# Optimization experiments

Hardware: AMD Instinct MI355X
Metric: run time of the kernel (lower is better)

The kernel has to match this reference:

```python
import jax, jax.numpy as jnp
import numpy as np

N_NODES = 100000
N_EDGES = 1250000
NUM_SKILLS = 100000
HID = 64


def _sage(h, src, dst, Wl, bl, Wr, n):
    # SAGEConv (PyG defaults): out = lin_l(mean_{j in N(i)} h_j) + lin_r(h_i)
    msgs = h[src]                                        # [E, d] gather
    agg = jax.ops.segment_sum(msgs, dst, num_segments=n)  # [N, d]
    cnt = jax.ops.segment_sum(jnp.ones((src.shape[0],), h.dtype), dst, num_segments=n)
    mean = agg / jnp.maximum(cnt, 1.0)[:, None]
    return mean @ Wl + bl + h @ Wr


def _prelu(v, a):
    return jnp.where(v >= 0, v, a * v)


def setup_inputs() -> dict:
    key = jax.random.key(0)
    ks = jax.random.split(key, 12)
    s = 1.0 / np.sqrt(HID)
    inp = {
        "x": jax.random.randint(ks[0], (N_NODES,), 0, NUM_SKILLS),
        "edge_index": jax.random.randint(ks[1], (2, N_EDGES), 0, N_NODES),
        "edge_weight": jax.random.uniform(ks[2], (N_EDGES,), jnp.float32),
        "emb": jax.random.normal(ks[3], (NUM_SKILLS, HID), jnp.float32),
        "Wl1": jax.random.uniform(ks[4], (HID, HID), jnp.float32, -s, s),
        "bl1": jnp.zeros((HID,), jnp.float32),
        "Wr1": jax.random.uniform(ks[5], (HID, HID), jnp.float32, -s, s),
        "a1": jnp.float32(0.25),
        "Wl2": jax.random.uniform(ks[6], (HID, HID), jnp.float32, -s, s),
        "bl2": jnp.zeros((HID,), jnp.float32),
        "Wr2": jax.random.uniform(ks[7], (HID, HID), jnp.float32, -s, s),
        "a2": jnp.float32(0.25),
        "Wout": jax.random.uniform(ks[8], (HID, HID), jnp.float32, -s, s),
        "bout": jnp.zeros((HID,), jnp.float32),
    }
    return inp


def reference(x, edge_index, edge_weight, emb, Wl1, bl1, Wr1, a1,
              Wl2, bl2, Wr2, a2, Wout, bout):
    src, dst = edge_index[0], edge_index[1]
    n = x.shape[0]
    h0 = emb[x]                                           # [N, d] embedding lookup
    h1 = _prelu(_sage(h0, src, dst, Wl1, bl1, Wr1, n), a1)  # dropout = identity (eval)
    h2 = _prelu(_sage(h1, src, dst, Wl2, bl2, Wr2, n), a2)
    return h2 @ Wout + bout
```

## Files before the change

### kernel.cpp

```cpp
#include <hip/hip_runtime.h>
#include <hip/hip_bf16.h>

#define N_NODES 100000
#define N_EDGES 1250000
#define HID 64
#define LDSS 72
#define NB 196
#define NBLOCK 128
#define EMB_BLOCKS 6250

typedef __bf16 bf16x8 __attribute__((ext_vector_type(8)));
typedef float  f32x4  __attribute__((ext_vector_type(4)));

__device__ __forceinline__ float bflo(uint u) {
    union { unsigned int i; float f; } v; v.i = u << 16; return v.f;
}
__device__ __forceinline__ float bfhi(uint u) {
    union { unsigned int i; float f; } v; v.i = u & 0xFFFF0000u; return v.f;
}
__device__ __forceinline__ ushort f2bf(float f) {
    union { float f; unsigned int i; } v; v.f = f;
    unsigned int x = v.i;
    return (ushort)((x + 0x7fffu + ((x >> 16) & 1u)) >> 16);
}

__global__ __launch_bounds__(256) void prep(const int* __restrict__ x,
                                            const float* __restrict__ emb,
                                            ushort* __restrict__ h0,
                                            const int* __restrict__ dst,
                                            int* __restrict__ gh,
                                            const float* __restrict__ Wl1,
                                            const float* __restrict__ Wr1,
                                            const float* __restrict__ Wl2,
                                            const float* __restrict__ Wr2,
                                            const float* __restrict__ Wout,
                                            ushort* __restrict__ wbf) {
    const int b = blockIdx.x;
    const int tid = threadIdx.x;
    if (b < EMB_BLOCKS) {
        int t = b * 256 + tid;
        int row = t >> 4, c = t & 15;
        int idx = x[row];
        float4 v = ((const float4*)(emb + (size_t)idx * HID))[c];
        ushort4 w;
        w.x = f2bf(v.x); w.y = f2bf(v.y); w.z = f2bf(v.z); w.w = f2bf(v.w);
        ((ushort4*)(h0 + (size_t)row * HID))[c] = w;
    } else if (b < EMB_BLOCKS + NBLOCK) {
        __shared__ int hist[NB];
        const int bb = b - EMB_BLOCKS;
        for (int i = tid; i < NB; i += 256) hist[i] = 0;
        __syncthreads();
        const int4* d4 = (const int4*)dst;
        for (int e = bb * 256 + tid; e < N_EDGES / 4; e += NBLOCK * 256) {
            int4 v = d4[e];
            atomicAdd(&hist[v.x >> 9], 1);
            atomicAdd(&hist[v.y >> 9], 1);
            atomicAdd(&hist[v.z >> 9], 1);
            atomicAdd(&hist[v.w >> 9], 1);
        }
        __syncthreads();
        for (int i = tid; i < NB; i += 256) gh[bb * NB + i] = hist[i];
    } else {
        const int wb = b - EMB_BLOCKS - NBLOCK;
        const float* W = (wb == 0) ? Wl1 : (wb == 1) ? Wr1 :
                         (wb == 2) ? Wl2 : (wb == 3) ? Wr2 : Wout;
        ushort* o = wbf + wb * 4096;
        for (int idx = tid; idx < 4096; idx += 256) {
            int k = idx >> 6, n = idx & 63;
            o[n * 64 + k] = f2bf(W[idx]);
        }
    }
}

__global__ __launch_bounds__(256) void p3_scatter(const int* __restrict__ src,
                                                  const int* __restrict__ dst,
                                                  const int* __restrict__ gh,
                                                  int* __restrict__ bstart,
                                                  uint* __restrict__ ebuf) {
    __shared__ int base[NB];
    __shared__ int run[NB];
    __shared__ int wsum[4];
    const int tid = threadIdx.x, lane = tid & 63, wave = tid >> 6;
    int myTot = 0, myPre = 0;
    if (tid < NB) {
        for (int b = 0; b < NBLOCK; ++b) {
            int c = gh[b * NB + tid];
            if (b == (int)blockIdx.x) myPre = myTot;
            myTot += c;
        }
    }
    int x = myTot;
#pragma unroll
    for (int d = 1; d < 64; d <<= 1) {
        int y = __shfl_up(x, d, 64);
        if (lane >= d) x += y;
    }
    if (lane == 63) wsum[wave] = x;
    __syncthreads();
    if (wave == 0) {
        int s = (lane < 4) ? wsum[lane] : 0;
#pragma unroll
        for (int d = 1; d < 4; d <<= 1) {
            int y = __shfl_up(s, d, 64);
            if (lane >= d) s += y;
        }
        if (lane < 4) wsum[lane] = s;
    }
    __syncthreads();
    int waveoff = (wave == 0) ? 0 : wsum[wave - 1];
    int excl = waveoff + (x - myTot);
    if (tid < NB) {
        base[tid] = excl + myPre;
        run[tid] = 0;
        if (blockIdx.x == 0) bstart[tid] = excl;
    }
    if (blockIdx.x == 0 && tid == 0) bstart[NB] = N_EDGES;
    __syncthreads();
    const int4* s4 = (const int4*)src;
    const int4* d4 = (const int4*)dst;
    for (int e = blockIdx.x * 256 + tid; e < N_EDGES / 4; e += NBLOCK * 256) {
        int4 dv = d4[e];
        int4 sv = s4[e];
        int b0 = dv.x >> 9;
        int r0 = atomicAdd(&run[b0], 1);
        ebuf[base[b0] + r0] = ((uint)(dv.x & 511) << 17) | (uint)sv.x;
        int b1 = dv.y >> 9;
        int r1 = atomicAdd(&run[b1], 1);
        ebuf[base[b1] + r1] = ((uint)(dv.y & 511) << 17) | (uint)sv.y;
        int b2 = dv.z >> 9;
        int r2 = atomicAdd(&run[b2], 1);
        ebuf[base[b2] + r2] = ((uint)(dv.z & 511) << 17) | (uint)sv.z;
        int b3 = dv.w >> 9;
        int r3 = atomicAdd(&run[b3], 1);
        ebuf[base[b3] + r3] = ((uint)(dv.w & 511) << 17) | (uint)sv.w;
    }
}

__global__ __launch_bounds__(256) void p4_csr(const uint* __restrict__ ebuf,
                                              const int* __restrict__ bstart,
                                              int* __restrict__ rowptr,
                                              int* __restrict__ csr_src) {
    __shared__ int hist[512], hoff[512], run[512];
    __shared__ int wsum[4];
    const int v = blockIdx.x;
    const int tid = threadIdx.x, lane = tid & 63, wave = tid >> 6;
    const int node0 = v << 9;
    const int nn = min(512, N_NODES - node0);
    const int beg = bstart[v], end = bstart[v + 1];

    for (int i = tid; i < 512; i += 256) { hist[i] = 0; run[i] = 0; }
    __syncthreads();
    for (int e = beg + tid; e < end; e += 256)
        atomicAdd(&hist[ebuf[e] >> 17], 1);
    __syncthreads();
    int h0 = hist[2 * tid], h1 = hist[2 * tid + 1];
    int s = h0 + h1;
    int x = s;
#pragma unroll
    for (int d = 1; d < 64; d <<= 1) {
        int y = __shfl_up(x, d, 64);
        if (lane >= d) x += y;
    }
    if (lane == 63) wsum[wave] = x;
    __syncthreads();
    if (wave == 0) {
        int s2 = (lane < 4) ? wsum[lane] : 0;
#pragma unroll
        for (int d = 1; d < 4; d <<= 1) {
            int y = __shfl_up(s2, d, 64);
            if (lane >= d) s2 += y;
        }
        if (lane < 4) wsum[lane] = s2;
    }
    __syncthreads();
    int waveoff = (wave == 0) ? 0 : wsum[wave - 1];
    int excl = waveoff + (x - s);
    hoff[2 * tid] = excl;
    hoff[2 * tid + 1] = excl + h0;
    __syncthreads();
    for (int j = tid; j < nn; j += 256) rowptr[node0 + j] = beg + hoff[j];
    if (v == NB - 1 && tid == 0) rowptr[N_NODES] = N_EDGES;
    for (int e = beg + tid; e < end; e += 256) {
        uint p = ebuf[e];
        int dl = p >> 17;
        int r = atomicAdd(&run[dl], 1);
        csr_src[beg + hoff[dl] + r] = (int)(p & 0x1FFFFu);
    }
}

#define ACCUM(wa, wb)                                                      \
    a0 += bflo(wa.x); a1 += bfhi(wa.x); a2 += bflo(wa.y); a3 += bfhi(wa.y); \
    a4 += bflo(wa.z); a5 += bfhi(wa.z); a6 += bflo(wa.w); a7 += bfhi(wa.w); \
    a8 += bflo(wb.x); a9 += bfhi(wb.x); a10 += bflo(wb.y); a11 += bfhi(wb.y); \
    a12 += bflo(wb.z); a13 += bfhi(wb.z); a14 += bflo(wb.w); a15 += bfhi(wb.w);

template <bool OUTPROJ>
__global__ __launch_bounds__(256, 4) void layer_fused(
    const int* __restrict__ rowptr, const int* __restrict__ csr_src,
    const ushort* __restrict__ hin,
    const ushort* __restrict__ wl_bf, const float* __restrict__ bl,
    const ushort* __restrict__ wr_bf, const float* __restrict__ alpha_p,
    const ushort* __restrict__ wo_bf, const float* __restrict__ bo,
    void* __restrict__ out_p) {
    __shared__ __align__(16) ushort sA[64][LDSS];

    const int tid = threadIdx.x;
    const int row0 = blockIdx.x * 64;

    const int g = tid >> 2, q = tid & 3;
    {
        int node = row0 + g;
        uint4 o0 = {0, 0, 0, 0}, o1 = {0, 0, 0, 0};
        if (node < N_NODES) {
            int beg = rowptr[node], end = rowptr[node + 1];
            float a0 = 0.f, a1 = 0.f, a2 = 0.f, a3 = 0.f;
            float a4 = 0.f, a5 = 0.f, a6 = 0.f, a7 = 0.f;
            float a8 = 0.f, a9 = 0.f, a10 = 0.f, a11 = 0.f;
            float a12 = 0.f, a13 = 0.f, a14 = 0.f, a15 = 0.f;
            int i = beg;
            for (; i + 4 <= end; i += 4) {
                int s0 = csr_src[i], s1 = csr_src[i + 1];
                int s2 = csr_src[i + 2], s3 = csr_src[i + 3];
                const uint4* p0 = (const uint4*)&hin[(size_t)s0 * HID + q * 16];
                const uint4* p1 = (const uint4*)&hin[(size_t)s1 * HID + q * 16];
                const uint4* p2 = (const uint4*)&hin[(size_t)s2 * HID + q * 16];
                const uint4* p3 = (const uint4*)&hin[(size_t)s3 * HID + q * 16];
                uint4 w0a = p0[0], w0b = p0[1];
                uint4 w1a = p1[0], w1b = p1[1];
                uint4 w2a = p2[0], w2b = p2[1];
                uint4 w3a = p3[0], w3b = p3[1];
                ACCUM(w0a, w0b)
                ACCUM(w1a, w1b)
                ACCUM(w2a, w2b)
                ACCUM(w3a, w3b)
            }
            for (; i < end; ++i) {
                int s0 = csr_src[i];
                const uint4* p0 = (const uint4*)&hin[(size_t)s0 * HID + q * 16];
                uint4 w0a = p0[0], w0b = p0[1];
                ACCUM(w0a, w0b)
            }
            float inv = (end > beg) ? 1.0f / (float)(end - beg) : 0.f;
            o0.x = (uint)f2bf(a0 * inv)  | ((uint)f2bf(a1 * inv) << 16);
            o0.y = (uint)f2bf(a2 * inv)  | ((uint)f2bf(a3 * inv) << 16);
            o0.z = (uint)f2bf(a4 * inv)  | ((uint)f2bf(a5 * inv) << 16);
            o0.w = (uint)f2bf(a6 * inv)  | ((uint)f2bf(a7 * inv) << 16);
            o1.x = (uint)f2bf(a8 * inv)  | ((uint)f2bf(a9 * inv) << 16);
            o1.y = (uint)f2bf(a10 * inv) | ((uint)f2bf(a11 * inv) << 16);
            o1.z = (uint)f2bf(a12 * inv) | ((uint)f2bf(a13 * inv) << 16);
            o1.w = (uint)f2bf(a14 * inv) | ((uint)f2bf(a15 * inv) << 16);
        }
        *(uint4*)&sA[g][q * 16] = o0;
        *(uint4*)&sA[g][q * 16 + 8] = o1;
    }

    const int wave = tid >> 6, lane = tid & 63;
    const int quad = lane >> 4, lr = lane & 15;
    const int r0 = wave * 16;
    const int grow = row0 + r0 + lr;
    const float alpha = alpha_p[0];

    bf16x8 hf[2], af[2];
#pragma unroll
    for (int ks = 0; ks < 2; ++ks) {
        int k0 = ks * 32 + quad * 8;
        uint4 hv = {0, 0, 0, 0};
        if (grow < N_NODES) hv = *(const uint4*)&hin[(size_t)grow * HID + k0];
        hf[ks] = __builtin_bit_cast(bf16x8, hv);
        uint4 av = *(const uint4*)&sA[r0 + lr][k0];
        af[ks] = __builtin_bit_cast(bf16x8, av);
    }

    f32x4 acc[4];
#pragma unroll
    for (int nt = 0; nt < 4; ++nt) {
        f32x4 a = {0.f, 0.f, 0.f, 0.f};
#pragma unroll
        for (int ks = 0; ks < 2; ++ks) {
            int k0 = ks * 32 + quad * 8;
            bf16x8 wr = *(const bf16x8*)&wr_bf[(nt * 16 + lr) * 64 + k0];
            a = __builtin_amdgcn_mfma_f32_16x16x32_bf16(hf[ks], wr, a, 0, 0, 0);
            bf16x8 wl = *(const bf16x8*)&wl_bf[(nt * 16 + lr) * 64 + k0];
            a = __builtin_amdgcn_mfma_f32_16x16x32_bf16(af[ks], wl, a, 0, 0, 0);
        }
        acc[nt] = a;
    }

    if constexpr (!OUTPROJ) {
#pragma unroll
        for (int nt = 0; nt < 4; ++nt) {
            int col = nt * 16 + lr;
            float bias = bl[col];
#pragma unroll
            for (int r = 0; r < 4; ++r) {
                int row = r0 + quad * 4 + r;
                float v = acc[nt][r] + bias;
                v = (v >= 0.f) ? v : alpha * v;
                sA[row][col] = f2bf(v);
            }
        }
        ushort* outp = (ushort*)out_p;
        const int lrow = lane >> 3, lch = lane & 7;
#pragma unroll
        for (int pass = 0; pass < 2; ++pass) {
            int row = r0 + pass * 8 + lrow;
            int gg2 = row0 + row;
            if (gg2 < N_NODES) {
                uint4 v4 = *(const uint4*)&sA[row][lch * 8];
                *(uint4*)&outp[(size_t)gg2 * HID + lch * 8] = v4;
            }
        }
    } else {
#pragma unroll
        for (int nt = 0; nt < 4; ++nt) {
            int col = nt * 16 + lr;
            float bias = bl[col];
#pragma unroll
            for (int r = 0; r < 4; ++r) {
                int row = r0 + quad * 4 + r;
                float v = acc[nt][r] + bias;
                v = (v >= 0.f) ? v : alpha * v;
                sA[row][col] = f2bf(v);
            }
        }
        bf16x8 h2f[2];
#pragma unroll
        for (int ks = 0; ks < 2; ++ks) {
            int k0 = ks * 32 + quad * 8;
            uint4 hv = *(const uint4*)&sA[r0 + lr][k0];
            h2f[ks] = __builtin_bit_cast(bf16x8, hv);
        }
        f32x4 acc2[4];
#pragma unroll
        for (int nt = 0; nt < 4; ++nt) {
            f32x4 a = {0.f, 0.f, 0.f, 0.f};
#pragma unroll
            for (int ks = 0; ks < 2; ++ks) {
                int k0 = ks * 32 + quad * 8;
                bf16x8 wo = *(const bf16x8*)&wo_bf[(nt * 16 + lr) * 64 + k0];
                a = __builtin_amdgcn_mfma_f32_16x16x32_bf16(h2f[ks], wo, a, 0, 0, 0);
            }
            acc2[nt] = a;
        }
        float* outp = (float*)out_p;
#pragma unroll
        for (int nt = 0; nt < 4; ++nt) {
            int col = nt * 16 + lr;
            float bias = bo[col];
#pragma unroll
            for (int r = 0; r < 4; ++r) {
                int row = r0 + quad * 4 + r;
                int gg2 = row0 + row;
                if (gg2 < N_NODES)
                    outp[(size_t)gg2 * HID + col] = acc2[nt][r] + bias;
            }
        }
    }
}

extern "C" void kernel_launch(void* const* d_in, const int* in_sizes, int n_in,
                              void* d_out, int out_size, void* d_ws, size_t ws_size,
                              hipStream_t stream) {
    const int*   x    = (const int*)d_in[0];
    const int*   src  = (const int*)d_in[1];
    const int*   dst  = src + N_EDGES;
    const float* emb  = (const float*)d_in[3];
    const float* Wl1  = (const float*)d_in[4];
    const float* bl1  = (const float*)d_in[5];
    const float* Wr1  = (const float*)d_in[6];
    const float* a1   = (const float*)d_in[7];
    const float* Wl2  = (const float*)d_in[8];
    const float* bl2  = (const float*)d_in[9];
    const float* Wr2  = (const float*)d_in[10];
    const float* a2   = (const float*)d_in[11];
    const float* Wout = (const float*)d_in[12];
    const float* bout = (const float*)d_in[13];

    char* ws = (char*)d_ws;
    int*    gh      = (int*)ws;
    int*    bstart  = (int*)(ws + 101248);
    int*    rowptr  = (int*)(ws + 102080);
    ushort* wbf     = (ushort*)(ws + 502144);
    uint*   ebuf    = (uint*)(ws + 543104);
    int*    csr_src = (int*)(ws + 5543104);
    ushort* h0      = (ushort*)(ws + 10543104);
    ushort* h1      = (ushort*)(ws + 23343104);

    ushort* wl1b  = wbf;
    ushort* wr1b  = wbf + 4096;
    ushort* wl2b  = wbf + 8192;
    ushort* wr2b  = wbf + 12288;
    ushort* woutb = wbf + 16384;

    const int gemm_blocks = (N_NODES + 63) / 64;

    prep<<<EMB_BLOCKS + NBLOCK + 5, 256, 0, stream>>>(
        x, emb, h0, dst, gh, Wl1, Wr1, Wl2, Wr2, Wout, wbf);
    p3_scatter<<<NBLOCK, 256, 0, stream>>>(src, dst, gh, bstart, ebuf);
    p4_csr<<<NB, 256, 0, stream>>>(ebuf, bstart, rowptr, csr_src);

    layer_fused<false><<<gemm_blocks, 256, 0, stream>>>(
        rowptr, csr_src, h0, wl1b, bl1, wr1b, a1, wr1b, bl1, h1);
    layer_fused<true><<<gemm_blocks, 256, 0, stream>>>(
        rowptr, csr_src, h1, wl2b, bl2, wr2b, a2, woutb, bout, d_out);
}
```

Baseline: 246.5 us.

## Stage neighbor-row gathers through swizzled LDS with wave-cooperative coalesced loads

The mean-aggregation gather in the fused layer kernel now has each wave load the contiguous edge range of its 16 nodes cooperatively. Every lane fetches 16 bytes of a neighbor row, and rows are written to a double-buffered, XOR-swizzled LDS staging area while the next chunk is prefetched. Threads then accumulate their own node's neighbors from LDS. This replaces per-thread irregular 32-byte loads with full-row coalesced gathers and overlaps loads with accumulation. In exchange it adds 32KB of LDS per block, lowers the occupancy hint from 4 to 3, and adds extra shuffles and LDS traffic. An unroll pragma is also added to the histogram prefix loop.

Measured after the change: 276.3 us. 12.1% more time.

```diff
diff --git a/kernel.cpp b/kernel.cpp
--- a/kernel.cpp
+++ b/kernel.cpp
@@ -83,6 +83,7 @@
     const int tid = threadIdx.x, lane = tid & 63, wave = tid >> 6;
     int myTot = 0, myPre = 0;
     if (tid < NB) {
+#pragma unroll 8
         for (int b = 0; b < NBLOCK; ++b) {
             int c = gh[b * NB + tid];
             if (b == (int)blockIdx.x) myPre = myTot;
@@ -195,7 +196,7 @@
     a12 += bflo(wb.z); a13 += bfhi(wb.z); a14 += bflo(wb.w); a15 += bfhi(wb.w);
 
 template <bool OUTPROJ>
-__global__ __launch_bounds__(256, 4) void layer_fused(
+__global__ __launch_bounds__(256, 3) void layer_fused(
     const int* __restrict__ rowptr, const int* __restrict__ csr_src,
     const ushort* __restrict__ hin,
     const ushort* __restrict__ wl_bf, const float* __restrict__ bl,
@@ -203,58 +204,91 @@
     const ushort* __restrict__ wo_bf, const float* __restrict__ bo,
     void* __restrict__ out_p) {
     __shared__ __align__(16) ushort sA[64][LDSS];
+    __shared__ __align__(16) uint stg[4][2][1024];
 
     const int tid = threadIdx.x;
     const int row0 = blockIdx.x * 64;
-
+    const int wave = tid >> 6, lane = tid & 63;
     const int g = tid >> 2, q = tid & 3;
+    const int erow = lane >> 3, epc = lane & 7;
+    const int wslot = (epc ^ erow) * 4;
+
     {
-        int node = row0 + g;
-        uint4 o0 = {0, 0, 0, 0}, o1 = {0, 0, 0, 0};
-        if (node < N_NODES) {
-            int beg = rowptr[node], end = rowptr[node + 1];
-            float a0 = 0.f, a1 = 0.f, a2 = 0.f, a3 = 0.f;
-            float a4 = 0.f, a5 = 0.f, a6 = 0.f, a7 = 0.f;
-            float a8 = 0.f, a9 = 0.f, a10 = 0.f, a11 = 0.f;
-            float a12 = 0.f, a13 = 0.f, a14 = 0.f, a15 = 0.f;
-            int i = beg;
-            for (; i + 4 <= end; i += 4) {
-                int s0 = csr_src[i], s1 = csr_src[i + 1];
-                int s2 = csr_src[i + 2], s3 = csr_src[i + 3];
-                const uint4* p0 = (const uint4*)&hin[(size_t)s0 * HID + q * 16];
-                const uint4* p1 = (const uint4*)&hin[(size_t)s1 * HID + q * 16];
-                const uint4* p2 = (const uint4*)&hin[(size_t)s2 * HID + q * 16];
-                const uint4* p3 = (const uint4*)&hin[(size_t)s3 * HID + q * 16];
-                uint4 w0a = p0[0], w0b = p0[1];
-                uint4 w1a = p1[0], w1b = p1[1];
-                uint4 w2a = p2[0], w2b = p2[1];
-                uint4 w3a = p3[0], w3b = p3[1];
-                ACCUM(w0a, w0b)
-                ACCUM(w1a, w1b)
-                ACCUM(w2a, w2b)
-                ACCUM(w3a, w3b)
-            }
-            for (; i < end; ++i) {
-                int s0 = csr_src[i];
-                const uint4* p0 = (const uint4*)&hin[(size_t)s0 * HID + q * 16];
-                uint4 w0a = p0[0], w0b = p0[1];
-                ACCUM(w0a, w0b)
-            }
-            float inv = (end > beg) ? 1.0f / (float)(end - beg) : 0.f;
-            o0.x = (uint)f2bf(a0 * inv)  | ((uint)f2bf(a1 * inv) << 16);
-            o0.y = (uint)f2bf(a2 * inv)  | ((uint)f2bf(a3 * inv) << 16);
-            o0.z = (uint)f2bf(a4 * inv)  | ((uint)f2bf(a5 * inv) << 16);
-            o0.w = (uint)f2bf(a6 * inv)  | ((uint)f2bf(a7 * inv) << 16);
-            o1.x = (uint)f2bf(a8 * inv)  | ((uint)f2bf(a9 * inv) << 16);
-            o1.y = (uint)f2bf(a10 * inv) | ((uint)f2bf(a11 * inv) << 16);
-            o1.z = (uint)f2bf(a12 * inv) | ((uint)f2bf(a13 * inv) << 16);
-            o1.w = (uint)f2bf(a14 * inv) | ((uint)f2bf(a15 * inv) << 16);
-        }
+        const int nbase = row0 + wave * 16;
+        int estart = 0, eend = 0;
+        if (nbase < N_NODES) {
+            estart = rowptr[nbase];
+            eend   = rowptr[min(nbase + 16, N_NODES)];
+        }
+        const int node = row0 + g;
+        int beg = 0, end = 0;
+        if (node < N_NODES) { beg = rowptr[node]; end = rowptr[node + 1]; }
+
+        float a0 = 0.f, a1 = 0.f, a2 = 0.f, a3 = 0.f;
+        float a4 = 0.f, a5 = 0.f, a6 = 0.f, a7 = 0.f;
+        float a8 = 0.f, a9 = 0.f, a10 = 0.f, a11 = 0.f;
+        float a12 = 0.f, a13 = 0.f, a14 = 0.f, a15 = 0.f;
+
+        const int nch = (eend - estart + 31) >> 5;
+        if (nch > 0) {
+            uint4 rA, rB, rC, rD;
+            {
+                int idxv = csr_src[min(estart + lane, eend - 1)];
+                int i0 = __shfl(idxv, erow, 64);
+                int i1 = __shfl(idxv, 8 + erow, 64);
+                int i2 = __shfl(idxv, 16 + erow, 64);
+                int i3 = __shfl(idxv, 24 + erow, 64);
+                rA = *(const uint4*)&hin[(size_t)i0 * HID + epc * 8];
+                rB = *(const uint4*)&hin[(size_t)i1 * HID + epc * 8];
+                rC = *(const uint4*)&hin[(size_t)i2 * HID + epc * 8];
+                rD = *(const uint4*)&hin[(size_t)i3 * HID + epc * 8];
+            }
+            for (int ch = 0; ch < nch; ++ch) {
+                uint* buf = &stg[wave][ch & 1][0];
+                int idxn = 0;
+                const bool more = (ch + 1 < nch);
+                if (more)
+                    idxn = csr_src[min(estart + (ch + 1) * 32 + lane, eend - 1)];
+                uint* w = buf + erow * 32 + wslot;
+                *(uint4*)(w)       = rA;
+                *(uint4*)(w + 256) = rB;
+                *(uint4*)(w + 512) = rC;
+                *(uint4*)(w + 768) = rD;
+                if (more) {
+                    int i0 = __shfl(idxn, erow, 64);
+                    int i1 = __shfl(idxn, 8 + erow, 64);
+                    int i2 = __shfl(idxn, 16 + erow, 64);
+                    int i3 = __shfl(idxn, 24 + erow, 64);
+                    rA = *(const uint4*)&hin[(size_t)i0 * HID + epc * 8];
+                    rB = *(const uint4*)&hin[(size_t)i1 * HID + epc * 8];
+                    rC = *(const uint4*)&hin[(size_t)i2 * HID + epc * 8];
+                    rD = *(const uint4*)&hin[(size_t)i3 * HID + epc * 8];
+                }
+                const int ch0 = estart + ch * 32;
+                int lo = max(beg, ch0), hi = min(end, ch0 + 32);
+                for (int e = lo; e < hi; ++e) {
+                    int rr = e - ch0;
+                    const uint* rbase = buf + rr * 32;
+                    uint4 wa = *(const uint4*)(rbase + (((2 * q)     ^ (rr & 7)) * 4));
+                    uint4 wb = *(const uint4*)(rbase + (((2 * q + 1) ^ (rr & 7)) * 4));
+                    ACCUM(wa, wb)
+                }
+            }
+        }
+        float inv = (end > beg) ? 1.0f / (float)(end - beg) : 0.f;
+        uint4 o0, o1;
+        o0.x = (uint)f2bf(a0 * inv)  | ((uint)f2bf(a1 * inv) << 16);
+        o0.y = (uint)f2bf(a2 * inv)  | ((uint)f2bf(a3 * inv) << 16);
+        o0.z = (uint)f2bf(a4 * inv)  | ((uint)f2bf(a5 * inv) << 16);
+        o0.w = (uint)f2bf(a6 * inv)  | ((uint)f2bf(a7 * inv) << 16);
+        o1.x = (uint)f2bf(a8 * inv)  | ((uint)f2bf(a9 * inv) << 16);
+        o1.y = (uint)f2bf(a10 * inv) | ((uint)f2bf(a11 * inv) << 16);
+        o1.z = (uint)f2bf(a12 * inv) | ((uint)f2bf(a13 * inv) << 16);
+        o1.w = (uint)f2bf(a14 * inv) | ((uint)f2bf(a15 * inv) << 16);
         *(uint4*)&sA[g][q * 16] = o0;
         *(uint4*)&sA[g][q * 16 + 8] = o1;
     }
 
-    const int wave = tid >> 6, lane = tid & 63;
     const int quad = lane >> 4, lr = lane & 15;
     const int r0 = wave * 16;
     const int grow = row0 + r0 + lr;
```
